# Performance work log

Hardware: AMD Instinct MI355X
Metric: run time of the kernel (lower is better)

The kernel has to match this reference:

```python
import jax, jax.numpy as jnp
import numpy as np

B, S, HID = 1, 2048, 3072
NH, NKV, HD = 24, 8, 128
ROT = 96
OP = NH * HD + 2 * NKV * HD
MASK_VALUE = -jnp.finfo(jnp.float32).max


def setup_inputs() -> dict:
    key = jax.random.key(0)
    k1, k2, k3, k4, k5 = jax.random.split(key, 5)
    hidden_states = jax.random.normal(k1, (B, S, HID), dtype=jnp.float32)
    # rotary embeddings: use actual cos/sin of rope angles for realism
    inv_freq = 1.0 / (10000.0 ** (jnp.arange(0, ROT, 2, dtype=jnp.float32) / ROT))
    t = jnp.arange(S, dtype=jnp.float32)
    freqs = jnp.outer(t, inv_freq)  # [S, ROT/2]
    emb = jnp.concatenate([freqs, freqs], axis=-1)  # [S, ROT]
    cos = jnp.broadcast_to(jnp.cos(emb)[None], (B, S, ROT))
    sin = jnp.broadcast_to(jnp.sin(emb)[None], (B, S, ROT))
    attention_mask = jnp.ones((B, S), dtype=bool)
    w_qkv = jax.random.normal(k2, (OP, HID), dtype=jnp.float32) * (HID ** -0.5)
    w_o = jax.random.normal(k3, (HID, HID), dtype=jnp.float32) * (HID ** -0.5)
    return {"hidden_states": hidden_states, "cos": cos, "sin": sin,
            "attention_mask": attention_mask, "w_qkv": w_qkv, "w_o": w_o}


def rotate_half(x):
    x1, x2 = jnp.split(x, 2, axis=-1)
    return jnp.concatenate([-x2, x1], axis=-1)


def apply_rope(q, k, cos, sin):
    # cos/sin: [B, S, ROT] -> [B, 1, S, ROT]
    cos = cos[:, None]
    sin = sin[:, None]
    rd = cos.shape[-1]
    q_rot, q_pass = q[..., :rd], q[..., rd:]
    k_rot, k_pass = k[..., :rd], k[..., rd:]
    q = jnp.concatenate([q_rot * cos + rotate_half(q_rot) * sin, q_pass], axis=-1)
    k = jnp.concatenate([k_rot * cos + rotate_half(k_rot) * sin, k_pass], axis=-1)
    return q, k


def reference(hidden_states, cos, sin, attention_mask, w_qkv, w_o):
    b, n, _ = hidden_states.shape
    qkv = hidden_states @ w_qkv.T  # [B, S, OP]
    q, k, v = jnp.split(qkv, [NH * HD, NH * HD + NKV * HD], axis=-1)
    # b n (h d) -> b h n d
    q = q.reshape(b, n, NH, HD).transpose(0, 2, 1, 3)
    k = k.reshape(b, n, NKV, HD).transpose(0, 2, 1, 3)
    v = v.reshape(b, n, NKV, HD).transpose(0, 2, 1, 3)
    q, k = apply_rope(q, k, cos, sin)
    q = q * (HD ** -0.5)
    n_rep = NH // NKV
    if n_rep > 1:
        k = jnp.repeat(k, n_rep, axis=1)
        v = jnp.repeat(v, n_rep, axis=1)
    sim = jnp.einsum('bhid,bhjd->bhij', q, k)
    causal = jnp.triu(jnp.ones((n, n), dtype=bool), k=1)
    sim = jnp.where(causal, MASK_VALUE, sim)
    sim = jnp.where(~attention_mask[:, None, None, :], MASK_VALUE, sim)
    attn = jax.nn.softmax(sim.astype(jnp.float32), axis=-1).astype(v.dtype)
    out = jnp.einsum('bhij,bhjd->bhid', attn, v)
    out = out.transpose(0, 2, 1, 3).reshape(b, n, NH * HD)  # b h n d -> b n (h d)
    return out @ w_o.T
```

## Files before the change

### kernel.cpp

```cpp
#include <hip/hip_runtime.h>

typedef unsigned short u16;
typedef unsigned int u32;
typedef __bf16 bf16x8 __attribute__((ext_vector_type(8)));
typedef float f32x4 __attribute__((ext_vector_type(4)));

#define S_LEN 2048
#define HIDDEN 3072
#define NHEADS 24
#define NKVH 8
#define HDIM 128
#define QKVW 5120
#define QKLD 4096
#define PSTR 80

__device__ __forceinline__ u16 f2bf(float f) {
  u32 u = __float_as_uint(f);
  u32 r = (u + 0x7fffu + ((u >> 16) & 1u)) >> 16;
  return (u16)r;
}
__device__ __forceinline__ float bf2f(u16 h) { return __uint_as_float(((u32)h) << 16); }

__device__ __forceinline__ void gload_lds16(const void* g, void* l) {
  __builtin_amdgcn_global_load_lds((const __attribute__((address_space(1))) void*)g,
                                   (__attribute__((address_space(3))) void*)l, 16, 0, 0);
}

__global__ void cast4(const float4* __restrict__ in, uint2* __restrict__ out, int n4) {
  int i = blockIdx.x * blockDim.x + threadIdx.x;
  if (i >= n4) return;
  float4 f = in[i];
  uint2 o;
  o.x = ((u32)f2bf(f.y) << 16) | f2bf(f.x);
  o.y = ((u32)f2bf(f.w) << 16) | f2bf(f.z);
  out[i] = o;
}

template <bool OUT_BF16, bool WRITE_VT>
__global__ __launch_bounds__(256) void gemm_bt(const u16* __restrict__ A, const u16* __restrict__ B,
                                               float* __restrict__ Cf, u16* __restrict__ Cb,
                                               u16* __restrict__ vtg,
                                               int M, int N, int K, int ldc) {
  __shared__ u16 As[128 * 32];
  __shared__ u16 Bs[128 * 32];
  const int tid = threadIdx.x;
  const int w = tid >> 6, lane = tid & 63;
  const int wm = w & 1, wn = w >> 1;
  const int l15 = lane & 15, qd = lane >> 4;
  const int m0 = blockIdx.y * 128, n0 = blockIdx.x * 128;
  const int rS = lane >> 2, cS = (lane & 3) * 8;
  f32x4 acc[4][4] = {};
  for (int k0 = 0; k0 < K; k0 += 32) {
    __syncthreads();
#pragma unroll
    for (int t = 0; t < 2; ++t) {
      int r = t * 64 + w * 16;
      gload_lds16(A + (size_t)(m0 + r + rS) * K + k0 + cS, &As[r * 32]);
      gload_lds16(B + (size_t)(n0 + r + rS) * K + k0 + cS, &Bs[r * 32]);
    }
    __syncthreads();
    bf16x8 af[4], bfm[4];
#pragma unroll
    for (int i = 0; i < 4; ++i) af[i] = *(const bf16x8*)&As[(wm * 64 + i * 16 + l15) * 32 + qd * 8];
#pragma unroll
    for (int j = 0; j < 4; ++j) bfm[j] = *(const bf16x8*)&Bs[(wn * 64 + j * 16 + l15) * 32 + qd * 8];
#pragma unroll
    for (int i = 0; i < 4; ++i)
#pragma unroll
      for (int j = 0; j < 4; ++j)
        acc[i][j] = __builtin_amdgcn_mfma_f32_16x16x32_bf16(af[i], bfm[j], acc[i][j], 0, 0, 0);
  }
  if (WRITE_VT && n0 >= 4096) {
#pragma unroll
    for (int i = 0; i < 4; ++i)
#pragma unroll
      for (int j = 0; j < 4; ++j) {
        int n = (n0 - 4096) + wn * 64 + j * 16 + l15;
        int m = m0 + wm * 64 + i * 16 + qd * 4;
        uint2 p;
        p.x = ((u32)f2bf(acc[i][j][1]) << 16) | f2bf(acc[i][j][0]);
        p.y = ((u32)f2bf(acc[i][j][3]) << 16) | f2bf(acc[i][j][2]);
        *(uint2*)&vtg[(size_t)n * S_LEN + m] = p;
      }
    return;
  }
#pragma unroll
  for (int i = 0; i < 4; ++i)
#pragma unroll
    for (int j = 0; j < 4; ++j)
#pragma unroll
      for (int r = 0; r < 4; ++r) {
        int m = m0 + wm * 64 + i * 16 + qd * 4 + r;
        int n = n0 + wn * 64 + j * 16 + l15;
        if (OUT_BF16) Cb[(size_t)m * ldc + n] = f2bf(acc[i][j][r]);
        else          Cf[(size_t)m * ldc + n] = acc[i][j][r];
      }
}

template <bool OUT_BF16>
__global__ __launch_bounds__(256) void gemm_bt64(const u16* __restrict__ A, const u16* __restrict__ B,
                                                 float* __restrict__ Cf, u16* __restrict__ Cb,
                                                 int M, int N, int K, int ldc) {
  __shared__ u16 As[64 * 32];
  __shared__ u16 Bs[128 * 32];
  const int tid = threadIdx.x;
  const int w = tid >> 6, lane = tid & 63;
  const int wm = w & 1, wn = w >> 1;
  const int l15 = lane & 15, qd = lane >> 4;
  const int m0 = blockIdx.y * 64, n0 = blockIdx.x * 128;
  const int rS = lane >> 2, cS = (lane & 3) * 8;
  f32x4 acc[2][4] = {};
  for (int k0 = 0; k0 < K; k0 += 32) {
    __syncthreads();
    gload_lds16(A + (size_t)(m0 + w * 16 + rS) * K + k0 + cS, &As[w * 16 * 32]);
#pragma unroll
    for (int t = 0; t < 2; ++t) {
      int r = t * 64 + w * 16;
      gload_lds16(B + (size_t)(n0 + r + rS) * K + k0 + cS, &Bs[r * 32]);
    }
    __syncthreads();
    bf16x8 af[2], bfm[4];
#pragma unroll
    for (int i = 0; i < 2; ++i) af[i] = *(const bf16x8*)&As[(wm * 32 + i * 16 + l15) * 32 + qd * 8];
#pragma unroll
    for (int j = 0; j < 4; ++j) bfm[j] = *(const bf16x8*)&Bs[(wn * 64 + j * 16 + l15) * 32 + qd * 8];
#pragma unroll
    for (int i = 0; i < 2; ++i)
#pragma unroll
      for (int j = 0; j < 4; ++j)
        acc[i][j] = __builtin_amdgcn_mfma_f32_16x16x32_bf16(af[i], bfm[j], acc[i][j], 0, 0, 0);
  }
#pragma unroll
  for (int i = 0; i < 2; ++i)
#pragma unroll
    for (int j = 0; j < 4; ++j)
#pragma unroll
      for (int r = 0; r < 4; ++r) {
        int m = m0 + wm * 32 + i * 16 + qd * 4 + r;
        int n = n0 + wn * 64 + j * 16 + l15;
        if (OUT_BF16) Cb[(size_t)m * ldc + n] = f2bf(acc[i][j][r]);
        else          Cf[(size_t)m * ldc + n] = acc[i][j][r];
      }
}

__global__ __launch_bounds__(128) void rope_kernel(u16* __restrict__ qkv,
                                                   const float* __restrict__ cosb,
                                                   const float* __restrict__ sinb) {
  const int s = blockIdx.x;
  const int hh = blockIdx.y;
  const int d = threadIdx.x;
  const bool isq = hh < NHEADS;
  const size_t base = (size_t)s * QKLD + (isq ? hh * HDIM : HIDDEN + (hh - NHEADS) * HDIM);
  const float scale = 0.08838834764831845f;
  if (d < 48) {
    float x1 = bf2f(qkv[base + d]), x2 = bf2f(qkv[base + d + 48]);
    float c1 = cosb[s * 96 + d], s1 = sinb[s * 96 + d];
    float c2 = cosb[s * 96 + d + 48], s2 = sinb[s * 96 + d + 48];
    float o1 = x1 * c1 - x2 * s1;
    float o2 = x2 * c2 + x1 * s2;
    if (isq) { o1 *= scale; o2 *= scale; }
    qkv[base + d] = f2bf(o1);
    qkv[base + d + 48] = f2bf(o2);
  } else if (d >= 96 && isq) {
    qkv[base + d] = f2bf(bf2f(qkv[base + d]) * scale);
  }
}

__global__ __launch_bounds__(256) void flash_kernel(const u16* __restrict__ qkv,
                                                    const u16* __restrict__ vtg,
                                                    u16* __restrict__ ao) {
  __shared__ u16 Ks[4][64 * 32];
  __shared__ u16 Vt[128 * PSTR];
  __shared__ u16 Ps[64 * PSTR];
  const int bid = blockIdx.x;
  const int g = bid & 255, kk3 = bid >> 8;
  const int rank = (kk3 == 1) ? (kk3 << 8) + (255 - g) : (kk3 << 8) + g;
  const int h = rank % NHEADS;
  const int qi = 31 - rank / NHEADS;
  const int q0 = qi * 64;
  const int hkv = h / 3;
  const int tid = threadIdx.x;
  const int w = tid >> 6, lane = tid & 63;
  const int l15 = lane & 15, qd = lane >> 4;
  const int rS = lane >> 2, cS = (lane & 3) * 8;

  bf16x8 qf[4];
#pragma unroll
  for (int kk = 0; kk < 4; ++kk)
    qf[kk] = *(const bf16x8*)&qkv[(size_t)(q0 + w * 16 + l15) * QKLD + h * HDIM + kk * 32 + qd * 8];

  f32x4 o[8] = {};
  float lrow[4] = {0.f, 0.f, 0.f, 0.f};

  const u16* vb = vtg + (size_t)hkv * HDIM * S_LEN;
  const int vd = tid >> 3;
  const int vkv = (tid & 7) * 8;

  for (int kv0 = 0; kv0 <= q0; kv0 += 64) {
    __syncthreads();
#pragma unroll
    for (int t = 0; t < 4; ++t)
      gload_lds16(qkv + (size_t)(kv0 + t * 16 + rS) * QKLD + HIDDEN + hkv * HDIM + w * 32 + cS,
                  &Ks[w][t * 16 * 32]);
#pragma unroll
    for (int it = 0; it < 4; ++it) {
      int d = it * 32 + vd;
      uint4 vv = *(const uint4*)&vb[(size_t)d * S_LEN + kv0 + vkv];
      *(uint4*)&Vt[d * PSTR + vkv] = vv;
    }
    __syncthreads();

    f32x4 sc[4] = {};
#pragma unroll
    for (int j = 0; j < 4; ++j)
#pragma unroll
      for (int kk = 0; kk < 4; ++kk) {
        bf16x8 kf = *(const bf16x8*)&Ks[kk][(j * 16 + l15) * 32 + qd * 8];
        sc[j] = __builtin_amdgcn_mfma_f32_16x16x32_bf16(qf[kk], kf, sc[j], 0, 0, 0);
      }

    if (kv0 == q0) {
#pragma unroll
      for (int j = 0; j < 4; ++j)
#pragma unroll
        for (int r = 0; r < 4; ++r) {
          int row = w * 16 + qd * 4 + r;
          int col = j * 16 + l15;
          if (col > row) sc[j][r] = -1.0e30f;
        }
    }

#pragma unroll
    for (int j = 0; j < 4; ++j)
#pragma unroll
      for (int r = 0; r < 4; ++r) sc[j][r] = __expf(sc[j][r]);
#pragma unroll
    for (int r = 0; r < 4; ++r)
      lrow[r] += (sc[0][r] + sc[1][r]) + (sc[2][r] + sc[3][r]);

#pragma unroll
    for (int j = 0; j < 4; ++j)
#pragma unroll
      for (int r = 0; r < 4; ++r)
        Ps[(w * 16 + qd * 4 + r) * PSTR + j * 16 + l15] = f2bf(sc[j][r]);
    asm volatile("s_waitcnt lgkmcnt(0)" ::: "memory");

    bf16x8 pf[2];
#pragma unroll
    for (int kk = 0; kk < 2; ++kk)
      pf[kk] = *(const bf16x8*)&Ps[(w * 16 + l15) * PSTR + kk * 32 + qd * 8];
#pragma unroll
    for (int jn = 0; jn < 8; ++jn)
#pragma unroll
      for (int kk = 0; kk < 2; ++kk) {
        bf16x8 vf = *(const bf16x8*)&Vt[(jn * 16 + l15) * PSTR + kk * 32 + qd * 8];
        o[jn] = __builtin_amdgcn_mfma_f32_16x16x32_bf16(pf[kk], vf, o[jn], 0, 0, 0);
      }
  }

  float rinv[4];
#pragma unroll
  for (int r = 0; r < 4; ++r) {
    float s = lrow[r];
#pragma unroll
    for (int d = 1; d < 16; d <<= 1) s += __shfl_xor(s, d, 64);
    rinv[r] = 1.0f / s;
  }
#pragma unroll
  for (int jn = 0; jn < 8; ++jn)
#pragma unroll
    for (int r = 0; r < 4; ++r) {
      int row = q0 + w * 16 + qd * 4 + r;
      ao[(size_t)row * HIDDEN + h * HDIM + jn * 16 + l15] = f2bf(o[jn][r] * rinv[r]);
    }
}

extern "C" void kernel_launch(void* const* d_in, const int* in_sizes, int n_in,
                              void* d_out, int out_size, void* d_ws, size_t ws_size,
                              hipStream_t stream) {
  (void)in_sizes; (void)n_in; (void)out_size; (void)ws_size;
  const float* hs   = (const float*)d_in[0];
  const float* cosb = (const float*)d_in[1];
  const float* sinb = (const float*)d_in[2];
  const float* wqkv = (const float*)d_in[4];
  const float* wo   = (const float*)d_in[5];
  float* out = (float*)d_out;
  char* ws = (char*)d_ws;

  u16* hB   = (u16*)ws;
  u16* wB   = (u16*)(ws + 12582912);
  u16* qkvB = (u16*)(ws + 44040192);
  u16* vtgB = (u16*)(ws + 60817408);
  u16* aoB  = hB;
  u16* woB  = wB;

  cast4<<<6144, 256, 0, stream>>>((const float4*)hs, (uint2*)hB, 1572864);
  cast4<<<15360, 256, 0, stream>>>((const float4*)wqkv, (uint2*)wB, 3932160);
  gemm_bt<true, true><<<dim3(40, 16), 256, 0, stream>>>(hB, wB, nullptr, qkvB, vtgB,
                                                        2048, QKVW, 3072, QKLD);
  cast4<<<9216, 256, 0, stream>>>((const float4*)wo, (uint2*)woB, 2359296);
  rope_kernel<<<dim3(2048, 32), 128, 0, stream>>>(qkvB, cosb, sinb);
  flash_kernel<<<768, 256, 0, stream>>>(qkvB, vtgB, aoB);
  gemm_bt64<false><<<dim3(24, 32), 256, 0, stream>>>(aoB, woB, out, nullptr,
                                                     2048, HIDDEN, 3072, HIDDEN);
}
```

Baseline: 397.0 us.

## Split flash attention KV range across waves with cross-wave output reduction

The flash kernel now gives each wave a strided slice of the KV sequence for all 64 query rows, instead of each wave owning 16 query rows and sharing KV tiles staged through LDS. K and V fragments are loaded straight from global memory into registers, which removes the per-iteration block barriers. At the end, partial outputs are reduced through LDS in a tree, and row sums are combined before normalisation. The cost is far more accumulator registers (occupancy capped at 2 blocks), repeated Q reloads from global memory, and bf16 rounding of the partial sums during the reduction.

```diff
diff --git a/kernel.cpp b/kernel.cpp
--- a/kernel.cpp
+++ b/kernel.cpp
@@ -12,7 +12,6 @@
 #define HDIM 128
 #define QKVW 5120
 #define QKLD 4096
-#define PSTR 80
 
 __device__ __forceinline__ u16 f2bf(float f) {
   u32 u = __float_as_uint(f);
@@ -166,12 +165,10 @@
   }
 }
 
-__global__ __launch_bounds__(256) void flash_kernel(const u16* __restrict__ qkv,
-                                                    const u16* __restrict__ vtg,
-                                                    u16* __restrict__ ao) {
-  __shared__ u16 Ks[4][64 * 32];
-  __shared__ u16 Vt[128 * PSTR];
-  __shared__ u16 Ps[64 * PSTR];
+__global__ __launch_bounds__(256, 2) void flash3(const u16* __restrict__ qkv,
+                                                 const u16* __restrict__ vtg,
+                                                 u16* __restrict__ ao) {
+  __shared__ char smem[33792];
   const int bid = blockIdx.x;
   const int g = bid & 255, kk3 = bid >> 8;
   const int rank = (kk3 == 1) ? (kk3 << 8) + (255 - g) : (kk3 << 8) + g;
@@ -182,97 +179,159 @@
   const int tid = threadIdx.x;
   const int w = tid >> 6, lane = tid & 63;
   const int l15 = lane & 15, qd = lane >> 4;
-  const int rS = lane >> 2, cS = (lane & 3) * 8;
-
-  bf16x8 qf[4];
-#pragma unroll
-  for (int kk = 0; kk < 4; ++kk)
-    qf[kk] = *(const bf16x8*)&qkv[(size_t)(q0 + w * 16 + l15) * QKLD + h * HDIM + kk * 32 + qd * 8];
-
-  f32x4 o[8] = {};
-  float lrow[4] = {0.f, 0.f, 0.f, 0.f};
-
+
+  u16* Psw = (u16*)(smem + w * 5120);
+  float* Ls = (float*)(smem + 32768);
+  const u16* kb = qkv + HIDDEN + hkv * HDIM;
   const u16* vb = vtg + (size_t)hkv * HDIM * S_LEN;
-  const int vd = tid >> 3;
-  const int vkv = (tid & 7) * 8;
-
-  for (int kv0 = 0; kv0 <= q0; kv0 += 64) {
-    __syncthreads();
-#pragma unroll
-    for (int t = 0; t < 4; ++t)
-      gload_lds16(qkv + (size_t)(kv0 + t * 16 + rS) * QKLD + HIDDEN + hkv * HDIM + w * 32 + cS,
-                  &Ks[w][t * 16 * 32]);
-#pragma unroll
-    for (int it = 0; it < 4; ++it) {
-      int d = it * 32 + vd;
-      uint4 vv = *(const uint4*)&vb[(size_t)d * S_LEN + kv0 + vkv];
-      *(uint4*)&Vt[d * PSTR + vkv] = vv;
-    }
-    __syncthreads();
-
-    f32x4 sc[4] = {};
-#pragma unroll
-    for (int j = 0; j < 4; ++j)
-#pragma unroll
-      for (int kk = 0; kk < 4; ++kk) {
-        bf16x8 kf = *(const bf16x8*)&Ks[kk][(j * 16 + l15) * 32 + qd * 8];
-        sc[j] = __builtin_amdgcn_mfma_f32_16x16x32_bf16(qf[kk], kf, sc[j], 0, 0, 0);
-      }
-
-    if (kv0 == q0) {
-#pragma unroll
-      for (int j = 0; j < 4; ++j)
+  const u16* qb = qkv + h * HDIM;
+
+  f32x4 oa[4][8] = {};
+  f32x4 lr[4] = {};
+
+  for (int kv0 = w * 32; kv0 <= q0 + 32; kv0 += 128) {
+    bf16x8 kf[2][4];
+#pragma unroll
+    for (int j = 0; j < 2; ++j)
+#pragma unroll
+      for (int kk = 0; kk < 4; ++kk)
+        kf[j][kk] = *(const bf16x8*)&kb[(size_t)(kv0 + j * 16 + l15) * QKLD + kk * 32 + qd * 8];
+    const bool domask = (kv0 + 31 > q0);
+
+#pragma unroll
+    for (int i = 0; i < 4; ++i) {
+      bf16x8 qfi[4];
+#pragma unroll
+      for (int kk = 0; kk < 4; ++kk)
+        qfi[kk] = *(const bf16x8*)&qb[(size_t)(q0 + i * 16 + l15) * QKLD + kk * 32 + qd * 8];
+      f32x4 sc[2] = {};
+#pragma unroll
+      for (int kk = 0; kk < 4; ++kk)
+#pragma unroll
+        for (int j = 0; j < 2; ++j)
+          sc[j] = __builtin_amdgcn_mfma_f32_16x16x32_bf16(qfi[kk], kf[j][kk], sc[j], 0, 0, 0);
+      if (domask) {
+#pragma unroll
+        for (int j = 0; j < 2; ++j)
+#pragma unroll
+          for (int r = 0; r < 4; ++r) {
+            int row = q0 + i * 16 + qd * 4 + r;
+            int col = kv0 + j * 16 + l15;
+            if (col > row) sc[j][r] = -1.0e30f;
+          }
+      }
+#pragma unroll
+      for (int j = 0; j < 2; ++j)
 #pragma unroll
         for (int r = 0; r < 4; ++r) {
-          int row = w * 16 + qd * 4 + r;
-          int col = j * 16 + l15;
-          if (col > row) sc[j][r] = -1.0e30f;
+          float p = __expf(sc[j][r]);
+          sc[j][r] = p;
+          lr[i][r] += p;
         }
-    }
-
-#pragma unroll
-    for (int j = 0; j < 4; ++j)
-#pragma unroll
-      for (int r = 0; r < 4; ++r) sc[j][r] = __expf(sc[j][r]);
-#pragma unroll
-    for (int r = 0; r < 4; ++r)
-      lrow[r] += (sc[0][r] + sc[1][r]) + (sc[2][r] + sc[3][r]);
-
-#pragma unroll
-    for (int j = 0; j < 4; ++j)
-#pragma unroll
-      for (int r = 0; r < 4; ++r)
-        Ps[(w * 16 + qd * 4 + r) * PSTR + j * 16 + l15] = f2bf(sc[j][r]);
-    asm volatile("s_waitcnt lgkmcnt(0)" ::: "memory");
-
-    bf16x8 pf[2];
-#pragma unroll
-    for (int kk = 0; kk < 2; ++kk)
-      pf[kk] = *(const bf16x8*)&Ps[(w * 16 + l15) * PSTR + kk * 32 + qd * 8];
+#pragma unroll
+      for (int j = 0; j < 2; ++j)
+#pragma unroll
+        for (int r = 0; r < 4; ++r)
+          Psw[(i * 16 + qd * 4 + r) * 40 + j * 16 + l15] = f2bf(sc[j][r]);
+    }
+
+    bf16x8 vf[8];
 #pragma unroll
     for (int jn = 0; jn < 8; ++jn)
-#pragma unroll
-      for (int kk = 0; kk < 2; ++kk) {
-        bf16x8 vf = *(const bf16x8*)&Vt[(jn * 16 + l15) * PSTR + kk * 32 + qd * 8];
-        o[jn] = __builtin_amdgcn_mfma_f32_16x16x32_bf16(pf[kk], vf, o[jn], 0, 0, 0);
-      }
-  }
-
-  float rinv[4];
-#pragma unroll
-  for (int r = 0; r < 4; ++r) {
-    float s = lrow[r];
-#pragma unroll
-    for (int d = 1; d < 16; d <<= 1) s += __shfl_xor(s, d, 64);
-    rinv[r] = 1.0f / s;
-  }
-#pragma unroll
-  for (int jn = 0; jn < 8; ++jn)
+      vf[jn] = *(const bf16x8*)&vb[(size_t)(jn * 16 + l15) * S_LEN + kv0 + qd * 8];
+
+#pragma unroll
+    for (int i = 0; i < 4; ++i) {
+      bf16x8 pf = *(const bf16x8*)&Psw[(i * 16 + l15) * 40 + qd * 8];
+#pragma unroll
+      for (int jn = 0; jn < 8; ++jn)
+        oa[i][jn] = __builtin_amdgcn_mfma_f32_16x16x32_bf16(pf, vf[jn], oa[i][jn], 0, 0, 0);
+    }
+  }
+
+#pragma unroll
+  for (int i = 0; i < 4; ++i)
 #pragma unroll
     for (int r = 0; r < 4; ++r) {
-      int row = q0 + w * 16 + qd * 4 + r;
-      ao[(size_t)row * HIDDEN + h * HDIM + jn * 16 + l15] = f2bf(o[jn][r] * rinv[r]);
-    }
+      float s = lr[i][r];
+#pragma unroll
+      for (int d = 1; d < 16; d <<= 1) s += __shfl_xor(s, d, 64);
+      lr[i][r] = s;
+    }
+  if (l15 == 0) {
+#pragma unroll
+    for (int i = 0; i < 4; ++i)
+#pragma unroll
+      for (int r = 0; r < 4; ++r) Ls[w * 64 + i * 16 + qd * 4 + r] = lr[i][r];
+  }
+  __syncthreads();
+
+  char* R0 = smem;
+  char* R1 = smem + 16384;
+  if (w == 1 || w == 3) {
+    char* R = (w == 1) ? R0 : R1;
+#pragma unroll
+    for (int i = 0; i < 4; ++i)
+#pragma unroll
+      for (int jn = 0; jn < 8; ++jn) {
+        uint2 p;
+        p.x = ((u32)f2bf(oa[i][jn][1]) << 16) | f2bf(oa[i][jn][0]);
+        p.y = ((u32)f2bf(oa[i][jn][3]) << 16) | f2bf(oa[i][jn][2]);
+        *(uint2*)(R + ((i * 8 + jn) * 64 + lane) * 8) = p;
+      }
+  }
+  __syncthreads();
+  if (w == 0 || w == 2) {
+    char* R = (w == 0) ? R0 : R1;
+#pragma unroll
+    for (int i = 0; i < 4; ++i)
+#pragma unroll
+      for (int jn = 0; jn < 8; ++jn) {
+        uint2 p = *(const uint2*)(R + ((i * 8 + jn) * 64 + lane) * 8);
+        oa[i][jn][0] += bf2f((u16)(p.x & 0xffff));
+        oa[i][jn][1] += bf2f((u16)(p.x >> 16));
+        oa[i][jn][2] += bf2f((u16)(p.y & 0xffff));
+        oa[i][jn][3] += bf2f((u16)(p.y >> 16));
+      }
+  }
+  __syncthreads();
+  if (w == 2) {
+#pragma unroll
+    for (int i = 0; i < 4; ++i)
+#pragma unroll
+      for (int jn = 0; jn < 8; ++jn) {
+        uint2 p;
+        p.x = ((u32)f2bf(oa[i][jn][1]) << 16) | f2bf(oa[i][jn][0]);
+        p.y = ((u32)f2bf(oa[i][jn][3]) << 16) | f2bf(oa[i][jn][2]);
+        *(uint2*)(R0 + ((i * 8 + jn) * 64 + lane) * 8) = p;
+      }
+  }
+  __syncthreads();
+  if (w == 0) {
+    float rinv[4][4];
+#pragma unroll
+    for (int i = 0; i < 4; ++i)
+#pragma unroll
+      for (int r = 0; r < 4; ++r) {
+        int row = i * 16 + qd * 4 + r;
+        rinv[i][r] = 1.0f / (Ls[row] + Ls[64 + row] + Ls[128 + row] + Ls[192 + row]);
+      }
+#pragma unroll
+    for (int i = 0; i < 4; ++i)
+#pragma unroll
+      for (int jn = 0; jn < 8; ++jn) {
+        uint2 p = *(const uint2*)(R0 + ((i * 8 + jn) * 64 + lane) * 8);
+        oa[i][jn][0] += bf2f((u16)(p.x & 0xffff));
+        oa[i][jn][1] += bf2f((u16)(p.x >> 16));
+        oa[i][jn][2] += bf2f((u16)(p.y & 0xffff));
+        oa[i][jn][3] += bf2f((u16)(p.y >> 16));
+#pragma unroll
+        for (int r = 0; r < 4; ++r) {
+          int row = q0 + i * 16 + qd * 4 + r;
+          ao[(size_t)row * HIDDEN + h * HDIM + jn * 16 + l15] = f2bf(oa[i][jn][r] * rinv[i][r]);
+        }
+      }
+  }
 }
 
 extern "C" void kernel_launch(void* const* d_in, const int* in_sizes, int n_in,
@@ -300,7 +359,7 @@
                                                         2048, QKVW, 3072, QKLD);
   cast4<<<9216, 256, 0, stream>>>((const float4*)wo, (uint2*)woB, 2359296);
   rope_kernel<<<dim3(2048, 32), 128, 0, stream>>>(qkvB, cosb, sinb);
-  flash_kernel<<<768, 256, 0, stream>>>(qkvB, vtgB, aoB);
+  flash3<<<768, 256, 0, stream>>>(qkvB, vtgB, aoB);
   gemm_bt64<false><<<dim3(24, 32), 256, 0, stream>>>(aoB, woB, out, nullptr,
                                                      2048, HIDDEN, 3072, HIDDEN);
 }
```

Measured after the change: 455.8 us. +14.8%, slower.

## Repartition flash attention so each wave owns a KV slice and loads K/V directly

Applied to the files above, without the earlier changes.

The flash kernel is restructured so each wave handles 16 KV columns for all 64 query rows (holding all Q fragments in registers) and 32 output dims, instead of 16 query rows across all KV. K and V fragments are read straight from global memory into registers, which removes the K/V shared-memory staging. P is exchanged through a smaller LDS buffer, and row sums are combined across waves at the end through LDS. This cuts LDS traffic and footprint and sets launch bounds for two blocks per CU, at the cost of more registers for Q, uncoalesced per-wave global loads, and two barriers per iteration.

```diff
diff --git a/kernel.cpp b/kernel.cpp
--- a/kernel.cpp
+++ b/kernel.cpp
@@ -12,7 +12,6 @@
 #define HDIM 128
 #define QKVW 5120
 #define QKLD 4096
-#define PSTR 80
 
 __device__ __forceinline__ u16 f2bf(float f) {
   u32 u = __float_as_uint(f);
@@ -166,12 +165,11 @@
   }
 }
 
-__global__ __launch_bounds__(256) void flash_kernel(const u16* __restrict__ qkv,
-                                                    const u16* __restrict__ vtg,
-                                                    u16* __restrict__ ao) {
-  __shared__ u16 Ks[4][64 * 32];
-  __shared__ u16 Vt[128 * PSTR];
-  __shared__ u16 Ps[64 * PSTR];
+__global__ __launch_bounds__(256, 2) void flash4(const u16* __restrict__ qkv,
+                                                 const u16* __restrict__ vtg,
+                                                 u16* __restrict__ ao) {
+  __shared__ u16 Ps[64 * 72];
+  __shared__ float Ls[4][64];
   const int bid = blockIdx.x;
   const int g = bid & 255, kk3 = bid >> 8;
   const int rank = (kk3 == 1) ? (kk3 << 8) + (255 - g) : (kk3 << 8) + g;
@@ -182,96 +180,101 @@
   const int tid = threadIdx.x;
   const int w = tid >> 6, lane = tid & 63;
   const int l15 = lane & 15, qd = lane >> 4;
-  const int rS = lane >> 2, cS = (lane & 3) * 8;
-
-  bf16x8 qf[4];
-#pragma unroll
-  for (int kk = 0; kk < 4; ++kk)
-    qf[kk] = *(const bf16x8*)&qkv[(size_t)(q0 + w * 16 + l15) * QKLD + h * HDIM + kk * 32 + qd * 8];
-
-  f32x4 o[8] = {};
-  float lrow[4] = {0.f, 0.f, 0.f, 0.f};
-
+
+  const u16* kb = qkv + HIDDEN + hkv * HDIM;
   const u16* vb = vtg + (size_t)hkv * HDIM * S_LEN;
-  const int vd = tid >> 3;
-  const int vkv = (tid & 7) * 8;
+
+  bf16x8 qf[4][4];
+#pragma unroll
+  for (int i = 0; i < 4; ++i)
+#pragma unroll
+    for (int kk = 0; kk < 4; ++kk)
+      qf[i][kk] = *(const bf16x8*)&qkv[(size_t)(q0 + i * 16 + l15) * QKLD + h * HDIM + kk * 32 + qd * 8];
+
+  f32x4 oa[4][2] = {};
+  f32x4 lr[4] = {};
 
   for (int kv0 = 0; kv0 <= q0; kv0 += 64) {
-    __syncthreads();
-#pragma unroll
-    for (int t = 0; t < 4; ++t)
-      gload_lds16(qkv + (size_t)(kv0 + t * 16 + rS) * QKLD + HIDDEN + hkv * HDIM + w * 32 + cS,
-                  &Ks[w][t * 16 * 32]);
-#pragma unroll
-    for (int it = 0; it < 4; ++it) {
-      int d = it * 32 + vd;
-      uint4 vv = *(const uint4*)&vb[(size_t)d * S_LEN + kv0 + vkv];
-      *(uint4*)&Vt[d * PSTR + vkv] = vv;
-    }
-    __syncthreads();
-
+    bf16x8 kf[4];
+#pragma unroll
+    for (int kk = 0; kk < 4; ++kk)
+      kf[kk] = *(const bf16x8*)&kb[(size_t)(kv0 + w * 16 + l15) * QKLD + kk * 32 + qd * 8];
     f32x4 sc[4] = {};
 #pragma unroll
-    for (int j = 0; j < 4; ++j)
-#pragma unroll
-      for (int kk = 0; kk < 4; ++kk) {
-        bf16x8 kf = *(const bf16x8*)&Ks[kk][(j * 16 + l15) * 32 + qd * 8];
-        sc[j] = __builtin_amdgcn_mfma_f32_16x16x32_bf16(qf[kk], kf, sc[j], 0, 0, 0);
-      }
-
+    for (int i = 0; i < 4; ++i)
+#pragma unroll
+      for (int kk = 0; kk < 4; ++kk)
+        sc[i] = __builtin_amdgcn_mfma_f32_16x16x32_bf16(qf[i][kk], kf[kk], sc[i], 0, 0, 0);
     if (kv0 == q0) {
-#pragma unroll
-      for (int j = 0; j < 4; ++j)
+      int col = q0 + w * 16 + l15;
+#pragma unroll
+      for (int i = 0; i < 4; ++i)
 #pragma unroll
         for (int r = 0; r < 4; ++r) {
-          int row = w * 16 + qd * 4 + r;
-          int col = j * 16 + l15;
-          if (col > row) sc[j][r] = -1.0e30f;
+          int row = q0 + i * 16 + qd * 4 + r;
+          if (col > row) sc[i][r] = -1.0e30f;
         }
     }
-
-#pragma unroll
-    for (int j = 0; j < 4; ++j)
-#pragma unroll
-      for (int r = 0; r < 4; ++r) sc[j][r] = __expf(sc[j][r]);
-#pragma unroll
-    for (int r = 0; r < 4; ++r)
-      lrow[r] += (sc[0][r] + sc[1][r]) + (sc[2][r] + sc[3][r]);
-
-#pragma unroll
-    for (int j = 0; j < 4; ++j)
+#pragma unroll
+    for (int i = 0; i < 4; ++i) {
+#pragma unroll
+      for (int r = 0; r < 4; ++r) {
+        float p = __expf(sc[i][r]);
+        sc[i][r] = p;
+        lr[i][r] += p;
+      }
 #pragma unroll
       for (int r = 0; r < 4; ++r)
-        Ps[(w * 16 + qd * 4 + r) * PSTR + j * 16 + l15] = f2bf(sc[j][r]);
-    asm volatile("s_waitcnt lgkmcnt(0)" ::: "memory");
-
-    bf16x8 pf[2];
-#pragma unroll
-    for (int kk = 0; kk < 2; ++kk)
-      pf[kk] = *(const bf16x8*)&Ps[(w * 16 + l15) * PSTR + kk * 32 + qd * 8];
-#pragma unroll
-    for (int jn = 0; jn < 8; ++jn)
-#pragma unroll
-      for (int kk = 0; kk < 2; ++kk) {
-        bf16x8 vf = *(const bf16x8*)&Vt[(jn * 16 + l15) * PSTR + kk * 32 + qd * 8];
-        o[jn] = __builtin_amdgcn_mfma_f32_16x16x32_bf16(pf[kk], vf, o[jn], 0, 0, 0);
-      }
-  }
-
-  float rinv[4];
-#pragma unroll
-  for (int r = 0; r < 4; ++r) {
-    float s = lrow[r];
-#pragma unroll
-    for (int d = 1; d < 16; d <<= 1) s += __shfl_xor(s, d, 64);
-    rinv[r] = 1.0f / s;
-  }
-#pragma unroll
-  for (int jn = 0; jn < 8; ++jn)
+        Ps[(i * 16 + qd * 4 + r) * 72 + w * 16 + l15] = f2bf(sc[i][r]);
+    }
+    __syncthreads();
+
+    bf16x8 vf[2][2];
+#pragma unroll
+    for (int jn = 0; jn < 2; ++jn)
+#pragma unroll
+      for (int kc = 0; kc < 2; ++kc)
+        vf[jn][kc] = *(const bf16x8*)&vb[(size_t)(w * 32 + jn * 16 + l15) * S_LEN + kv0 + kc * 32 + qd * 8];
+#pragma unroll
+    for (int i = 0; i < 4; ++i) {
+      bf16x8 pf0 = *(const bf16x8*)&Ps[(i * 16 + l15) * 72 + qd * 8];
+      bf16x8 pf1 = *(const bf16x8*)&Ps[(i * 16 + l15) * 72 + 32 + qd * 8];
+#pragma unroll
+      for (int jn = 0; jn < 2; ++jn) {
+        oa[i][jn] = __builtin_amdgcn_mfma_f32_16x16x32_bf16(pf0, vf[jn][0], oa[i][jn], 0, 0, 0);
+        oa[i][jn] = __builtin_amdgcn_mfma_f32_16x16x32_bf16(pf1, vf[jn][1], oa[i][jn], 0, 0, 0);
+      }
+    }
+    __syncthreads();
+  }
+
+#pragma unroll
+  for (int i = 0; i < 4; ++i)
 #pragma unroll
     for (int r = 0; r < 4; ++r) {
-      int row = q0 + w * 16 + qd * 4 + r;
-      ao[(size_t)row * HIDDEN + h * HDIM + jn * 16 + l15] = f2bf(o[jn][r] * rinv[r]);
+      float s = lr[i][r];
+#pragma unroll
+      for (int d = 1; d < 16; d <<= 1) s += __shfl_xor(s, d, 64);
+      lr[i][r] = s;
+    }
+  if (l15 == 0) {
+#pragma unroll
+    for (int i = 0; i < 4; ++i)
+#pragma unroll
+      for (int r = 0; r < 4; ++r) Ls[w][i * 16 + qd * 4 + r] = lr[i][r];
+  }
+  __syncthreads();
+
+#pragma unroll
+  for (int i = 0; i < 4; ++i)
+#pragma unroll
+    for (int r = 0; r < 4; ++r) {
+      int row = i * 16 + qd * 4 + r;
+      float rinv = 1.0f / (Ls[0][row] + Ls[1][row] + Ls[2][row] + Ls[3][row]);
+#pragma unroll
+      for (int jn = 0; jn < 2; ++jn)
+        ao[(size_t)(q0 + row) * HIDDEN + h * HDIM + w * 32 + jn * 16 + l15] =
+            f2bf(oa[i][jn][r] * rinv);
     }
 }
 
@@ -300,7 +303,7 @@
                                                         2048, QKVW, 3072, QKLD);
   cast4<<<9216, 256, 0, stream>>>((const float4*)wo, (uint2*)woB, 2359296);
   rope_kernel<<<dim3(2048, 32), 128, 0, stream>>>(qkvB, cosb, sinb);
-  flash_kernel<<<768, 256, 0, stream>>>(qkvB, vtgB, aoB);
+  flash4<<<768, 256, 0, stream>>>(qkvB, vtgB, aoB);
   gemm_bt64<false><<<dim3(24, 32), 256, 0, stream>>>(aoB, woB, out, nullptr,
                                                      2048, HIDDEN, 3072, HIDDEN);
 }
```

New measurement: 419.6 us. +5.7%, slower.
